# Kernel optimization log

Hardware: AMD Instinct MI355X
Metric: run time of the kernel (lower is better)

## Reference

```python
import jax, jax.numpy as jnp
import numpy as np

T, B, V, L = 512, 32, 512, 128
NEG = -1e9  # safe -inf surrogate (keeps logaddexp gradients finite)


def setup_inputs() -> dict:
    key = jax.random.key(0)
    k1, k2, k3 = jax.random.split(key, 3)
    log_probs = jax.nn.log_softmax(
        jax.random.normal(k1, (T, B, V), dtype=jnp.float32), axis=-1)
    # ASG transition parameter (init ones in the module; use small noise for a
    # non-degenerate reference). transition[i, j] = score of j -> i.
    transition = 0.1 * jax.random.normal(k2, (V, V), dtype=jnp.float32)
    targets = jax.random.randint(k3, (B, L), 0, V)
    input_lengths = jnp.full((B,), T, dtype=jnp.int32)
    target_lengths = jnp.full((B,), L, dtype=jnp.int32)
    return {"log_probs": log_probs, "transition": transition,
            "targets": targets, "input_lengths": input_lengths,
            "target_lengths": target_lengths}


def _fcc(log_probs, transition, input_lengths):
    """Fully-connected criterion: log-partition over all label paths. [B]"""
    def step(alpha, lp_t):  # alpha, lp_t: [B, V]
        # alpha'[b, i] = lp_t[b, i] + logsumexp_j(alpha[b, j] + trans[i, j])
        alpha = lp_t + jax.nn.logsumexp(
            alpha[:, None, :] + transition[None, :, :], axis=2)
        return alpha, jax.nn.logsumexp(alpha, axis=1)

    a0 = log_probs[0]
    _, tail = jax.lax.scan(step, a0, log_probs[1:])
    scores = jnp.concatenate(
        [jax.nn.logsumexp(a0, axis=1)[None], tail], axis=0)  # [T, B]
    return scores[input_lengths - 1, jnp.arange(scores.shape[1])]


def _fac(log_probs, transition, targets, input_lengths, target_lengths):
    """Forced-alignment criterion: DP constrained to the target label seq. [B]"""
    Tt, Bb, _ = log_probs.shape
    Ll = targets.shape[1]
    trans_self = transition[targets, targets]                    # [B, L] stay
    trans_prev = transition[targets[:, 1:], targets[:, :-1]]     # [B, L-1] advance
    # emit[t, b, s] = log_probs[t, b, targets[b, s]]
    emit = jnp.take_along_axis(
        log_probs, jnp.broadcast_to(targets[None], (Tt, Bb, Ll)), axis=2)

    sel = (target_lengths - 1)[:, None]  # [B, 1]

    def final_of(beta):
        return jnp.take_along_axis(beta, sel, axis=1)[:, 0]

    beta0 = jnp.where(jnp.arange(Ll)[None, :] == 0, emit[0], NEG)  # [B, L]

    def step(beta, em_t):
        stay = beta + trans_self
        move = jnp.concatenate(
            [jnp.full((Bb, 1), NEG, beta.dtype),
             beta[:, :-1] + trans_prev], axis=1)
        beta = em_t + jnp.logaddexp(stay, move)
        return beta, final_of(beta)

    _, tail = jax.lax.scan(step, beta0, emit[1:])
    fins = jnp.concatenate([final_of(beta0)[None], tail], axis=0)  # [T, B]
    return fins[input_lengths - 1, jnp.arange(Bb)]


def reference(log_probs, transition, targets, input_lengths, target_lengths):
    # ASG loss (reduction='none'): FCC - FAC, shape [B]
    fcc = _fcc(log_probs, transition, input_lengths)
    fac = _fac(log_probs, transition, targets, input_lengths, target_lengths)
    return fcc - fac
```

## Files before the change

### kernel.cpp

```cpp
#include <hip/hip_runtime.h>
#include <stdint.h>

#define T_ 512
#define B_ 32
#define V_ 512
#define L_ 128
#define NEGF (-1000000000.0f)

#define SE_Q 69.0f
#define SU_Q 127.0f
#define LOGC 9.078313f

typedef int v4i __attribute__((ext_vector_type(4)));

template <int CTRL>
__device__ __forceinline__ int dppmov(int old_, int src) {
    return __builtin_amdgcn_update_dpp(old_, src, CTRL, 0xF, 0xF, false);
}
__device__ __forceinline__ float wave_max64(float x) {
    int xi = __float_as_int(x);
    x = fmaxf(x, __int_as_float(dppmov<0x111>(xi, xi))); xi = __float_as_int(x);
    x = fmaxf(x, __int_as_float(dppmov<0x112>(xi, xi))); xi = __float_as_int(x);
    x = fmaxf(x, __int_as_float(dppmov<0x114>(xi, xi))); xi = __float_as_int(x);
    x = fmaxf(x, __int_as_float(dppmov<0x118>(xi, xi))); xi = __float_as_int(x);
    x = fmaxf(x, __int_as_float(dppmov<0x142>(xi, xi))); xi = __float_as_int(x);
    x = fmaxf(x, __int_as_float(dppmov<0x143>(xi, xi)));
    return x;
}
__device__ __forceinline__ float wave_sum64(float x) {
    int xi = __float_as_int(x);
    x = x + __int_as_float(dppmov<0x111>(xi, xi)); xi = __float_as_int(x);
    x = x + __int_as_float(dppmov<0x112>(xi, xi)); xi = __float_as_int(x);
    x = x + __int_as_float(dppmov<0x114>(xi, xi)); xi = __float_as_int(x);
    x = x + __int_as_float(dppmov<0x118>(xi, xi)); xi = __float_as_int(x);
    x = x + __int_as_float(dppmov<0x142>(xi, xi)); xi = __float_as_int(x);
    x = x + __int_as_float(dppmov<0x143>(xi, xi));
    return x;
}
__device__ __forceinline__ unsigned fkey(float f) {
    unsigned u = __float_as_uint(f);
    return (u & 0x80000000u) ? ~u : (u | 0x80000000u);
}
__device__ __forceinline__ float funkey(unsigned k) {
    unsigned u = (k & 0x80000000u) ? (k ^ 0x80000000u) : ~k;
    return __uint_as_float(u);
}
__device__ __forceinline__ int sel4(v4i a, int r) {
    int x0 = (r & 1) ? a.y : a.x;
    int x1 = (r & 1) ? a.w : a.z;
    return (r & 2) ? x1 : x0;
}

__global__ void asg_prep(const float* __restrict__ trans, uint32_t* __restrict__ Et) {
    int o = blockIdx.x * blockDim.x + threadIdx.x;
    int d    = o & 3;
    int tid  = (o >> 2) & 511;
    int qreg = o >> 11;
    int tt = qreg >> 3, kt = qreg & 7;
    int w = tid >> 6, lane = tid & 63;
    int q = lane >> 4, n = lane & 15;
    int m  = 64 * w + 16 * tt + n;
    int k0 = 64 * kt + 16 * q + 4 * d;
    const float* tp = trans + (size_t)m * V_ + k0;
    uint32_t q0 = (uint32_t)fminf(127.0f, __expf(tp[0]) * SE_Q + 0.5f);
    uint32_t q1 = (uint32_t)fminf(127.0f, __expf(tp[1]) * SE_Q + 0.5f);
    uint32_t q2 = (uint32_t)fminf(127.0f, __expf(tp[2]) * SE_Q + 0.5f);
    uint32_t q3 = (uint32_t)fminf(127.0f, __expf(tp[3]) * SE_Q + 0.5f);
    Et[(size_t)o] = q0 | (q1 << 8) | (q2 << 16) | (q3 << 24);
}

__global__ __attribute__((amdgpu_flat_work_group_size(512, 512),
                          amdgpu_waves_per_eu(2, 2)))
void asg_main(
    const float* __restrict__ lp, const uint32_t* __restrict__ Et,
    const float* __restrict__ trans, const int* __restrict__ targets,
    const int* __restrict__ ilen, const int* __restrict__ tlen,
    float* __restrict__ fcc_ws, float* __restrict__ fac_ws)
{
    __shared__ float facb[256];
    __shared__ __align__(16) uint32_t u_lds[128];
    __shared__ __align__(16) float mw_lds[8];
    __shared__ unsigned mslotE;
    __shared__ float sumf;

    const int bb  = blockIdx.x;
    const int tid = threadIdx.x;

    if (bb < B_) {
        const int b    = bb;
        const int lane = tid & 63;
        const int w    = tid >> 6;
        const int q    = lane >> 4;
        const int n    = lane & 15;
        const int tt_o = n >> 2;
        const int rg_o = n & 3;
        const int i    = 64 * w + 16 * tt_o + 4 * q + rg_o;
        const int Tlen = ilen[b];

        uint4 er4[32];
        {
            const uint4* Eq = (const uint4*)Et;
            #pragma unroll
            for (int t8 = 0; t8 < 32; ++t8) er4[t8] = Eq[t8 * 512 + tid];
        }

        float alpha = lp[(size_t)b * V_ + i];
        float lpv   = lp[(size_t)1 * (B_ * V_) + (size_t)b * V_ + i];
        if (tid == 0) { mslotE = 0u; sumf = 0.0f; }
        __syncthreads();

        for (int t = 1; t < Tlen; ++t) {
            {
                float mx = wave_max64(alpha);
                if (lane == 63) mw_lds[w] = mx;
            }
            __syncthreads();

            float4 m0 = *(const float4*)&mw_lds[0];
            float4 m1 = *(const float4*)&mw_lds[4];
            float m = fmaxf(fmaxf(fmaxf(m0.x, m0.y), fmaxf(m0.z, m0.w)),
                            fmaxf(fmaxf(m1.x, m1.y), fmaxf(m1.z, m1.w)));

            {
                float u = __expf(alpha - m);
                uint32_t qu = (uint32_t)(u * SU_Q + 0.5f);
                int pv = (int)(qu << (8 * (i & 3)));
                pv |= dppmov<0xB1>(pv, pv);
                pv |= dppmov<0x4E>(pv, pv);
                if ((i & 3) == 0) u_lds[i >> 2] = (uint32_t)pv;
            }
            __syncthreads();

            uint4 bf[8];
            #pragma unroll
            for (int kt = 0; kt < 8; ++kt)
                bf[kt] = *(const uint4*)((const char*)u_lds + 64 * kt + 16 * q);

            int tn = (t + 1 < Tlen) ? (t + 1) : t;
            float lpv_n = lp[(size_t)tn * (B_ * V_) + (size_t)b * V_ + i];

            v4i a0, a1, a2, a3;
            {
                v4i z = {0, 0, 0, 0};
                a0 = z; a1 = z; a2 = z; a3 = z;
            }
            #pragma unroll
            for (int kt = 0; kt < 8; ++kt) {
                v4i bv = __builtin_bit_cast(v4i, bf[kt]);
                a0 = __builtin_amdgcn_mfma_i32_16x16x64_i8(
                        __builtin_bit_cast(v4i, er4[0 * 8 + kt]), bv, a0, 0, 0, 0);
                a1 = __builtin_amdgcn_mfma_i32_16x16x64_i8(
                        __builtin_bit_cast(v4i, er4[1 * 8 + kt]), bv, a1, 0, 0, 0);
                a2 = __builtin_amdgcn_mfma_i32_16x16x64_i8(
                        __builtin_bit_cast(v4i, er4[2 * 8 + kt]), bv, a2, 0, 0, 0);
                a3 = __builtin_amdgcn_mfma_i32_16x16x64_i8(
                        __builtin_bit_cast(v4i, er4[3 * 8 + kt]), bv, a3, 0, 0, 0);
            }

            int s0 = sel4(a0, rg_o), s1 = sel4(a1, rg_o);
            int s2 = sel4(a2, rg_o), s3 = sel4(a3, rg_o);
            int y0 = (tt_o & 1) ? s1 : s0;
            int y1 = (tt_o & 1) ? s3 : s2;
            int acc = (tt_o & 2) ? y1 : y0;

            alpha = lpv + (m - LOGC) + __logf((float)acc);
            lpv = lpv_n;
        }

        {
            float mx = wave_max64(alpha);
            if (lane == 63) atomicMax(&mslotE, fkey(mx));
        }
        __syncthreads();
        float m2 = funkey(mslotE);
        {
            float sv = wave_sum64(__expf(alpha - m2));
            if (lane == 63) atomicAdd(&sumf, sv);
        }
        __syncthreads();
        if (tid == 0) fcc_ws[b] = m2 + __logf(sumf);
    } else {
        const int b = bb - B_;
        const int l = tid;
        const bool active = (l < L_);
        const int Tlen = ilen[b];
        const int Llen = tlen[b];

        const int tl  = active ? targets[b * L_ + l] : 0;
        const int tlm = (active && l > 0) ? targets[b * L_ + l - 1] : 0;
        const float ts = active ? trans[(size_t)tl * V_ + tl] : 0.0f;
        const float tp = (active && l > 0) ? trans[(size_t)tl * V_ + tlm] : 0.0f;

        float beta = (l == 0) ? lp[(size_t)b * V_ + tl] : NEGF;
        float em_next = active ? lp[(size_t)1 * (B_ * V_) + (size_t)b * V_ + tl] : 0.0f;

        for (int t = 1; t < Tlen; ++t) {
            float* buf = facb + (t & 1) * L_;
            if (active) buf[l] = beta;
            __syncthreads();
            float prev = (active && l > 0) ? buf[l - 1] : NEGF;
            float em = em_next;
            if (active && t + 1 < Tlen)
                em_next = lp[(size_t)(t + 1) * (B_ * V_) + (size_t)b * V_ + tl];
            if (active) {
                float st = beta + ts;
                float mv = prev + tp;
                float mx = fmaxf(st, mv);
                float mn = fminf(st, mv);
                beta = em + mx + log1pf(__expf(mn - mx));
            }
        }
        if (active && l == Llen - 1) fac_ws[b] = beta;
    }
}

__global__ void asg_combine(const float* __restrict__ fcc_ws,
                            const float* __restrict__ fac_ws,
                            float* __restrict__ out) {
    int i = threadIdx.x;
    if (i < B_) out[i] = fcc_ws[i] - fac_ws[i];
}

extern "C" void kernel_launch(void* const* d_in, const int* in_sizes, int n_in,
                              void* d_out, int out_size, void* d_ws, size_t ws_size,
                              hipStream_t stream) {
    const float* lp      = (const float*)d_in[0];
    const float* trans   = (const float*)d_in[1];
    const int*   targets = (const int*)d_in[2];
    const int*   ilen    = (const int*)d_in[3];
    const int*   tlen    = (const int*)d_in[4];
    float* out = (float*)d_out;

    uint32_t* Et     = (uint32_t*)d_ws;
    float*    fcc_ws = (float*)((char*)d_ws + 65536 * 4);
    float*    fac_ws = fcc_ws + B_;

    hipLaunchKernelGGL(asg_prep, dim3(256), dim3(256), 0, stream, trans, Et);
    hipLaunchKernelGGL(asg_main, dim3(2 * B_), dim3(512), 0, stream,
                       lp, Et, trans, targets, ilen, tlen, fcc_ws, fac_ws);
    hipLaunchKernelGGL(asg_combine, dim3(1), dim3(64), 0, stream, fcc_ws, fac_ws, out);
}
```

Before: 550.4 us.

## Run FCC recurrence in linear domain, fuse transition quantization, bpermute own k-tile

```diff
diff --git a/kernel.cpp b/kernel.cpp
--- a/kernel.cpp
+++ b/kernel.cpp
@@ -51,28 +51,10 @@
     return (r & 2) ? x1 : x0;
 }
 
-__global__ void asg_prep(const float* __restrict__ trans, uint32_t* __restrict__ Et) {
-    int o = blockIdx.x * blockDim.x + threadIdx.x;
-    int d    = o & 3;
-    int tid  = (o >> 2) & 511;
-    int qreg = o >> 11;
-    int tt = qreg >> 3, kt = qreg & 7;
-    int w = tid >> 6, lane = tid & 63;
-    int q = lane >> 4, n = lane & 15;
-    int m  = 64 * w + 16 * tt + n;
-    int k0 = 64 * kt + 16 * q + 4 * d;
-    const float* tp = trans + (size_t)m * V_ + k0;
-    uint32_t q0 = (uint32_t)fminf(127.0f, __expf(tp[0]) * SE_Q + 0.5f);
-    uint32_t q1 = (uint32_t)fminf(127.0f, __expf(tp[1]) * SE_Q + 0.5f);
-    uint32_t q2 = (uint32_t)fminf(127.0f, __expf(tp[2]) * SE_Q + 0.5f);
-    uint32_t q3 = (uint32_t)fminf(127.0f, __expf(tp[3]) * SE_Q + 0.5f);
-    Et[(size_t)o] = q0 | (q1 << 8) | (q2 << 16) | (q3 << 24);
-}
-
 __global__ __attribute__((amdgpu_flat_work_group_size(512, 512),
                           amdgpu_waves_per_eu(2, 2)))
 void asg_main(
-    const float* __restrict__ lp, const uint32_t* __restrict__ Et,
+    const float* __restrict__ lp,
     const float* __restrict__ trans, const int* __restrict__ targets,
     const int* __restrict__ ilen, const int* __restrict__ tlen,
     float* __restrict__ fcc_ws, float* __restrict__ fac_ws)
@@ -98,43 +80,74 @@
         const int Tlen = ilen[b];
 
         uint4 er4[32];
-        {
-            const uint4* Eq = (const uint4*)Et;
+        #pragma unroll
+        for (int tt = 0; tt < 4; ++tt) {
             #pragma unroll
-            for (int t8 = 0; t8 < 32; ++t8) er4[t8] = Eq[t8 * 512 + tid];
-        }
-
-        float alpha = lp[(size_t)b * V_ + i];
-        float lpv   = lp[(size_t)1 * (B_ * V_) + (size_t)b * V_ + i];
+            for (int s = 0; s < 8; ++s) {
+                int kt = (w + s) & 7;
+                const float* tp = trans + (size_t)(64 * w + 16 * tt + n) * V_
+                                        + 64 * kt + 16 * q;
+                uint32_t dw[4];
+                #pragma unroll
+                for (int d = 0; d < 4; ++d) {
+                    float4 tv = *(const float4*)(tp + 4 * d);
+                    uint32_t c0 = (uint32_t)fminf(127.0f, __expf(tv.x) * SE_Q + 0.5f);
+                    uint32_t c1 = (uint32_t)fminf(127.0f, __expf(tv.y) * SE_Q + 0.5f);
+                    uint32_t c2 = (uint32_t)fminf(127.0f, __expf(tv.z) * SE_Q + 0.5f);
+                    uint32_t c3 = (uint32_t)fminf(127.0f, __expf(tv.w) * SE_Q + 0.5f);
+                    dw[d] = c0 | (c1 << 8) | (c2 << 16) | (c3 << 24);
+                }
+                er4[tt * 8 + s].x = dw[0]; er4[tt * 8 + s].y = dw[1];
+                er4[tt * 8 + s].z = dw[2]; er4[tt * 8 + s].w = dw[3];
+            }
+        }
+
+        float lpv0 = lp[(size_t)b * V_ + i];
+        float elp  = __expf(lpv0);
+        float lpv  = lp[(size_t)(B_ * V_) + (size_t)b * V_ + i];
+        float accf = 1.0f;
+        float S    = 0.0f;
         if (tid == 0) { mslotE = 0u; sumf = 0.0f; }
         __syncthreads();
 
         for (int t = 1; t < Tlen; ++t) {
-            {
-                float mx = wave_max64(alpha);
+            float key = elp * accf;
+            float elp_n = __expf(lpv);
+
+            {
+                float mx = wave_max64(key);
                 if (lane == 63) mw_lds[w] = mx;
             }
             __syncthreads();
 
             float4 m0 = *(const float4*)&mw_lds[0];
             float4 m1 = *(const float4*)&mw_lds[4];
-            float m = fmaxf(fmaxf(fmaxf(m0.x, m0.y), fmaxf(m0.z, m0.w)),
-                            fmaxf(fmaxf(m1.x, m1.y), fmaxf(m1.z, m1.w)));
-
-            {
-                float u = __expf(alpha - m);
-                uint32_t qu = (uint32_t)(u * SU_Q + 0.5f);
-                int pv = (int)(qu << (8 * (i & 3)));
+            float kmax = fmaxf(fmaxf(fmaxf(m0.x, m0.y), fmaxf(m0.z, m0.w)),
+                               fmaxf(fmaxf(m1.x, m1.y), fmaxf(m1.z, m1.w)));
+            float r127 = 127.0f * __builtin_amdgcn_rcpf(kmax);
+
+            int pv;
+            {
+                uint32_t qu = (uint32_t)fminf(127.0f, fmaf(key, r127, 0.5f));
+                pv = (int)(qu << (8 * (i & 3)));
                 pv |= dppmov<0xB1>(pv, pv);
                 pv |= dppmov<0x4E>(pv, pv);
                 if ((i & 3) == 0) u_lds[i >> 2] = (uint32_t)pv;
             }
+
+            int bbase = lane & 48;
+            int ox = __builtin_amdgcn_ds_bpermute(bbase +   0, pv);
+            int oy = __builtin_amdgcn_ds_bpermute(bbase +  64, pv);
+            int oz = __builtin_amdgcn_ds_bpermute(bbase + 128, pv);
+            int ow = __builtin_amdgcn_ds_bpermute(bbase + 192, pv);
             __syncthreads();
 
-            uint4 bf[8];
+            uint4 bfr[7];
             #pragma unroll
-            for (int kt = 0; kt < 8; ++kt)
-                bf[kt] = *(const uint4*)((const char*)u_lds + 64 * kt + 16 * q);
+            for (int s = 1; s < 8; ++s) {
+                int kt = (w + s) & 7;
+                bfr[s - 1] = *(const uint4*)((const char*)u_lds + 64 * kt + 16 * q);
+            }
 
             int tn = (t + 1 < Tlen) ? (t + 1) : t;
             float lpv_n = lp[(size_t)tn * (B_ * V_) + (size_t)b * V_ + i];
@@ -144,17 +157,28 @@
                 v4i z = {0, 0, 0, 0};
                 a0 = z; a1 = z; a2 = z; a3 = z;
             }
+            {
+                v4i bv; bv.x = ox; bv.y = oy; bv.z = oz; bv.w = ow;
+                a0 = __builtin_amdgcn_mfma_i32_16x16x64_i8(
+                        __builtin_bit_cast(v4i, er4[0]),  bv, a0, 0, 0, 0);
+                a1 = __builtin_amdgcn_mfma_i32_16x16x64_i8(
+                        __builtin_bit_cast(v4i, er4[8]),  bv, a1, 0, 0, 0);
+                a2 = __builtin_amdgcn_mfma_i32_16x16x64_i8(
+                        __builtin_bit_cast(v4i, er4[16]), bv, a2, 0, 0, 0);
+                a3 = __builtin_amdgcn_mfma_i32_16x16x64_i8(
+                        __builtin_bit_cast(v4i, er4[24]), bv, a3, 0, 0, 0);
+            }
             #pragma unroll
-            for (int kt = 0; kt < 8; ++kt) {
-                v4i bv = __builtin_bit_cast(v4i, bf[kt]);
+            for (int s = 1; s < 8; ++s) {
+                v4i bv = __builtin_bit_cast(v4i, bfr[s - 1]);
                 a0 = __builtin_amdgcn_mfma_i32_16x16x64_i8(
-                        __builtin_bit_cast(v4i, er4[0 * 8 + kt]), bv, a0, 0, 0, 0);
+                        __builtin_bit_cast(v4i, er4[0 * 8 + s]), bv, a0, 0, 0, 0);
                 a1 = __builtin_amdgcn_mfma_i32_16x16x64_i8(
-                        __builtin_bit_cast(v4i, er4[1 * 8 + kt]), bv, a1, 0, 0, 0);
+                        __builtin_bit_cast(v4i, er4[1 * 8 + s]), bv, a1, 0, 0, 0);
                 a2 = __builtin_amdgcn_mfma_i32_16x16x64_i8(
-                        __builtin_bit_cast(v4i, er4[2 * 8 + kt]), bv, a2, 0, 0, 0);
+                        __builtin_bit_cast(v4i, er4[2 * 8 + s]), bv, a2, 0, 0, 0);
                 a3 = __builtin_amdgcn_mfma_i32_16x16x64_i8(
-                        __builtin_bit_cast(v4i, er4[3 * 8 + kt]), bv, a3, 0, 0, 0);
+                        __builtin_bit_cast(v4i, er4[3 * 8 + s]), bv, a3, 0, 0, 0);
             }
 
             int s0 = sel4(a0, rg_o), s1 = sel4(a1, rg_o);
@@ -163,10 +187,13 @@
             int y1 = (tt_o & 1) ? s3 : s2;
             int acc = (tt_o & 2) ? y1 : y0;
 
-            alpha = lpv + (m - LOGC) + __logf((float)acc);
+            accf = (float)acc;
+            S += __logf(kmax) - LOGC;
+            elp = elp_n;
             lpv = lpv_n;
         }
 
+        float alpha = ((Tlen > 1) ? lpv : lpv0) + S + __logf(accf);
         {
             float mx = wave_max64(alpha);
             if (lane == 63) atomicMax(&mslotE, fkey(mx));
@@ -231,12 +258,10 @@
     const int*   tlen    = (const int*)d_in[4];
     float* out = (float*)d_out;
 
-    uint32_t* Et     = (uint32_t*)d_ws;
-    float*    fcc_ws = (float*)((char*)d_ws + 65536 * 4);
-    float*    fac_ws = fcc_ws + B_;
-
-    hipLaunchKernelGGL(asg_prep, dim3(256), dim3(256), 0, stream, trans, Et);
+    float* fcc_ws = (float*)d_ws;
+    float* fac_ws = fcc_ws + B_;
+
     hipLaunchKernelGGL(asg_main, dim3(2 * B_), dim3(512), 0, stream,
-                       lp, Et, trans, targets, ilen, tlen, fcc_ws, fac_ws);
+                       lp, trans, targets, ilen, tlen, fcc_ws, fac_ws);
     hipLaunchKernelGGL(asg_combine, dim3(1), dim3(64), 0, stream, fcc_ws, fac_ws, out);
 }
```

Measured after the change: 615.8 us. 1.12x slower.

## Halve FCC workgroup to four waves, each handling two states

Applied to the files above, without the earlier changes.

```diff
diff --git a/kernel.cpp b/kernel.cpp
--- a/kernel.cpp
+++ b/kernel.cpp
@@ -45,21 +45,16 @@
     unsigned u = (k & 0x80000000u) ? (k ^ 0x80000000u) : ~k;
     return __uint_as_float(u);
 }
-__device__ __forceinline__ int sel4(v4i a, int r) {
-    int x0 = (r & 1) ? a.y : a.x;
-    int x1 = (r & 1) ? a.w : a.z;
-    return (r & 2) ? x1 : x0;
-}
 
 __global__ void asg_prep(const float* __restrict__ trans, uint32_t* __restrict__ Et) {
     int o = blockIdx.x * blockDim.x + threadIdx.x;
     int d    = o & 3;
-    int tid  = (o >> 2) & 511;
-    int qreg = o >> 11;
+    int tid  = (o >> 2) & 255;
+    int qreg = o >> 10;
     int tt = qreg >> 3, kt = qreg & 7;
     int w = tid >> 6, lane = tid & 63;
     int q = lane >> 4, n = lane & 15;
-    int m  = 64 * w + 16 * tt + n;
+    int m  = 128 * w + 16 * tt + n;
     int k0 = 64 * kt + 16 * q + 4 * d;
     const float* tp = trans + (size_t)m * V_ + k0;
     uint32_t q0 = (uint32_t)fminf(127.0f, __expf(tp[0]) * SE_Q + 0.5f);
@@ -69,8 +64,8 @@
     Et[(size_t)o] = q0 | (q1 << 8) | (q2 << 16) | (q3 << 24);
 }
 
-__global__ __attribute__((amdgpu_flat_work_group_size(512, 512),
-                          amdgpu_waves_per_eu(2, 2)))
+__global__ __attribute__((amdgpu_flat_work_group_size(256, 256),
+                          amdgpu_waves_per_eu(1, 1)))
 void asg_main(
     const float* __restrict__ lp, const uint32_t* __restrict__ Et,
     const float* __restrict__ trans, const int* __restrict__ targets,
@@ -79,7 +74,7 @@
 {
     __shared__ float facb[256];
     __shared__ __align__(16) uint32_t u_lds[128];
-    __shared__ __align__(16) float mw_lds[8];
+    __shared__ __align__(16) float mw_lds[4];
     __shared__ unsigned mslotE;
     __shared__ float sumf;
 
@@ -92,42 +87,43 @@
         const int w    = tid >> 6;
         const int q    = lane >> 4;
         const int n    = lane & 15;
-        const int tt_o = n >> 2;
-        const int rg_o = n & 3;
-        const int i    = 64 * w + 16 * tt_o + 4 * q + rg_o;
+        const int tt_o = n >> 1;
+        const int i0   = 128 * w + 16 * tt_o + 4 * q + 2 * (n & 1);
         const int Tlen = ilen[b];
 
-        uint4 er4[32];
+        uint4 er[64];
         {
             const uint4* Eq = (const uint4*)Et;
             #pragma unroll
-            for (int t8 = 0; t8 < 32; ++t8) er4[t8] = Eq[t8 * 512 + tid];
-        }
-
-        float alpha = lp[(size_t)b * V_ + i];
-        float lpv   = lp[(size_t)1 * (B_ * V_) + (size_t)b * V_ + i];
+            for (int j = 0; j < 64; ++j) er[j] = Eq[j * 256 + tid];
+        }
+
+        float2 a0v = *(const float2*)&lp[(size_t)b * V_ + i0];
+        float alpha0 = a0v.x, alpha1 = a0v.y;
+        float2 lv = *(const float2*)&lp[(size_t)(B_ * V_) + (size_t)b * V_ + i0];
+        float lpv0 = lv.x, lpv1 = lv.y;
         if (tid == 0) { mslotE = 0u; sumf = 0.0f; }
         __syncthreads();
 
         for (int t = 1; t < Tlen; ++t) {
             {
-                float mx = wave_max64(alpha);
+                float mx = wave_max64(fmaxf(alpha0, alpha1));
                 if (lane == 63) mw_lds[w] = mx;
             }
             __syncthreads();
 
-            float4 m0 = *(const float4*)&mw_lds[0];
-            float4 m1 = *(const float4*)&mw_lds[4];
-            float m = fmaxf(fmaxf(fmaxf(m0.x, m0.y), fmaxf(m0.z, m0.w)),
-                            fmaxf(fmaxf(m1.x, m1.y), fmaxf(m1.z, m1.w)));
+            float4 mq = *(const float4*)&mw_lds[0];
+            float m = fmaxf(fmaxf(mq.x, mq.y), fmaxf(mq.z, mq.w));
 
             {
-                float u = __expf(alpha - m);
-                uint32_t qu = (uint32_t)(u * SU_Q + 0.5f);
-                int pv = (int)(qu << (8 * (i & 3)));
-                pv |= dppmov<0xB1>(pv, pv);
-                pv |= dppmov<0x4E>(pv, pv);
-                if ((i & 3) == 0) u_lds[i >> 2] = (uint32_t)pv;
+                float u0 = __expf(alpha0 - m);
+                float u1 = __expf(alpha1 - m);
+                uint32_t q0 = (uint32_t)(u0 * SU_Q + 0.5f);
+                uint32_t q1 = (uint32_t)(u1 * SU_Q + 0.5f);
+                int u16o = (int)(q0 | (q1 << 8));
+                int pr = dppmov<0xB1>(u16o, u16o);
+                if ((n & 1) == 0)
+                    u_lds[32 * w + 4 * (n >> 1) + q] = (uint32_t)(u16o | (pr << 16));
             }
             __syncthreads();
 
@@ -137,44 +133,68 @@
                 bf[kt] = *(const uint4*)((const char*)u_lds + 64 * kt + 16 * q);
 
             int tn = (t + 1 < Tlen) ? (t + 1) : t;
-            float lpv_n = lp[(size_t)tn * (B_ * V_) + (size_t)b * V_ + i];
-
-            v4i a0, a1, a2, a3;
+            float2 lvn = *(const float2*)&lp[(size_t)tn * (B_ * V_) + (size_t)b * V_ + i0];
+
+            v4i A0, A1, A2, A3, A4, A5, A6, A7;
             {
                 v4i z = {0, 0, 0, 0};
-                a0 = z; a1 = z; a2 = z; a3 = z;
+                A0 = z; A1 = z; A2 = z; A3 = z; A4 = z; A5 = z; A6 = z; A7 = z;
             }
             #pragma unroll
             for (int kt = 0; kt < 8; ++kt) {
                 v4i bv = __builtin_bit_cast(v4i, bf[kt]);
-                a0 = __builtin_amdgcn_mfma_i32_16x16x64_i8(
-                        __builtin_bit_cast(v4i, er4[0 * 8 + kt]), bv, a0, 0, 0, 0);
-                a1 = __builtin_amdgcn_mfma_i32_16x16x64_i8(
-                        __builtin_bit_cast(v4i, er4[1 * 8 + kt]), bv, a1, 0, 0, 0);
-                a2 = __builtin_amdgcn_mfma_i32_16x16x64_i8(
-                        __builtin_bit_cast(v4i, er4[2 * 8 + kt]), bv, a2, 0, 0, 0);
-                a3 = __builtin_amdgcn_mfma_i32_16x16x64_i8(
-                        __builtin_bit_cast(v4i, er4[3 * 8 + kt]), bv, a3, 0, 0, 0);
-            }
-
-            int s0 = sel4(a0, rg_o), s1 = sel4(a1, rg_o);
-            int s2 = sel4(a2, rg_o), s3 = sel4(a3, rg_o);
-            int y0 = (tt_o & 1) ? s1 : s0;
-            int y1 = (tt_o & 1) ? s3 : s2;
-            int acc = (tt_o & 2) ? y1 : y0;
-
-            alpha = lpv + (m - LOGC) + __logf((float)acc);
-            lpv = lpv_n;
+                A0 = __builtin_amdgcn_mfma_i32_16x16x64_i8(
+                        __builtin_bit_cast(v4i, er[0 * 8 + kt]), bv, A0, 0, 0, 0);
+                A1 = __builtin_amdgcn_mfma_i32_16x16x64_i8(
+                        __builtin_bit_cast(v4i, er[1 * 8 + kt]), bv, A1, 0, 0, 0);
+                A2 = __builtin_amdgcn_mfma_i32_16x16x64_i8(
+                        __builtin_bit_cast(v4i, er[2 * 8 + kt]), bv, A2, 0, 0, 0);
+                A3 = __builtin_amdgcn_mfma_i32_16x16x64_i8(
+                        __builtin_bit_cast(v4i, er[3 * 8 + kt]), bv, A3, 0, 0, 0);
+                A4 = __builtin_amdgcn_mfma_i32_16x16x64_i8(
+                        __builtin_bit_cast(v4i, er[4 * 8 + kt]), bv, A4, 0, 0, 0);
+                A5 = __builtin_amdgcn_mfma_i32_16x16x64_i8(
+                        __builtin_bit_cast(v4i, er[5 * 8 + kt]), bv, A5, 0, 0, 0);
+                A6 = __builtin_amdgcn_mfma_i32_16x16x64_i8(
+                        __builtin_bit_cast(v4i, er[6 * 8 + kt]), bv, A6, 0, 0, 0);
+                A7 = __builtin_amdgcn_mfma_i32_16x16x64_i8(
+                        __builtin_bit_cast(v4i, er[7 * 8 + kt]), bv, A7, 0, 0, 0);
+            }
+
+            const bool nb = (n & 1) != 0;
+            int p00 = nb ? A0.z : A0.x, p10 = nb ? A0.w : A0.y;
+            int p01 = nb ? A1.z : A1.x, p11 = nb ? A1.w : A1.y;
+            int p02 = nb ? A2.z : A2.x, p12 = nb ? A2.w : A2.y;
+            int p03 = nb ? A3.z : A3.x, p13 = nb ? A3.w : A3.y;
+            int p04 = nb ? A4.z : A4.x, p14 = nb ? A4.w : A4.y;
+            int p05 = nb ? A5.z : A5.x, p15 = nb ? A5.w : A5.y;
+            int p06 = nb ? A6.z : A6.x, p16 = nb ? A6.w : A6.y;
+            int p07 = nb ? A7.z : A7.x, p17 = nb ? A7.w : A7.y;
+            const bool t0b = (tt_o & 1) != 0;
+            const bool t1b = (tt_o & 2) != 0;
+            const bool t2b = (tt_o & 4) != 0;
+            int q00 = t0b ? p01 : p00, q01 = t0b ? p03 : p02;
+            int q02 = t0b ? p05 : p04, q03 = t0b ? p07 : p06;
+            int q10 = t0b ? p11 : p10, q11 = t0b ? p13 : p12;
+            int q12 = t0b ? p15 : p14, q13 = t0b ? p17 : p16;
+            int r00 = t1b ? q01 : q00, r01 = t1b ? q03 : q02;
+            int r10 = t1b ? q11 : q10, r11 = t1b ? q13 : q12;
+            int acc0 = t2b ? r01 : r00;
+            int acc1 = t2b ? r11 : r10;
+
+            alpha0 = lpv0 + (m - LOGC) + __logf((float)acc0);
+            alpha1 = lpv1 + (m - LOGC) + __logf((float)acc1);
+            lpv0 = lvn.x; lpv1 = lvn.y;
         }
 
         {
-            float mx = wave_max64(alpha);
+            float mx = wave_max64(fmaxf(alpha0, alpha1));
             if (lane == 63) atomicMax(&mslotE, fkey(mx));
         }
         __syncthreads();
         float m2 = funkey(mslotE);
         {
-            float sv = wave_sum64(__expf(alpha - m2));
+            float sv = wave_sum64(__expf(alpha0 - m2) + __expf(alpha1 - m2));
             if (lane == 63) atomicAdd(&sumf, sv);
         }
         __syncthreads();
@@ -236,7 +256,7 @@
     float*    fac_ws = fcc_ws + B_;
 
     hipLaunchKernelGGL(asg_prep, dim3(256), dim3(256), 0, stream, trans, Et);
-    hipLaunchKernelGGL(asg_main, dim3(2 * B_), dim3(512), 0, stream,
+    hipLaunchKernelGGL(asg_main, dim3(2 * B_), dim3(256), 0, stream,
                        lp, Et, trans, targets, ilen, tlen, fcc_ws, fac_ws);
     hipLaunchKernelGGL(asg_combine, dim3(1), dim3(64), 0, stream, fcc_ws, fac_ws, out);
 }
```

Result: slower. 682.6 us (+24.0%).

## Fuse prep, main and combine kernels into one launch with global flag sync

Applied to the files above, without the earlier changes.

```diff
diff --git a/kernel.cpp b/kernel.cpp
--- a/kernel.cpp
+++ b/kernel.cpp
@@ -51,31 +51,19 @@
     return (r & 2) ? x1 : x0;
 }
 
-__global__ void asg_prep(const float* __restrict__ trans, uint32_t* __restrict__ Et) {
-    int o = blockIdx.x * blockDim.x + threadIdx.x;
-    int d    = o & 3;
-    int tid  = (o >> 2) & 511;
-    int qreg = o >> 11;
-    int tt = qreg >> 3, kt = qreg & 7;
-    int w = tid >> 6, lane = tid & 63;
-    int q = lane >> 4, n = lane & 15;
-    int m  = 64 * w + 16 * tt + n;
-    int k0 = 64 * kt + 16 * q + 4 * d;
-    const float* tp = trans + (size_t)m * V_ + k0;
-    uint32_t q0 = (uint32_t)fminf(127.0f, __expf(tp[0]) * SE_Q + 0.5f);
-    uint32_t q1 = (uint32_t)fminf(127.0f, __expf(tp[1]) * SE_Q + 0.5f);
-    uint32_t q2 = (uint32_t)fminf(127.0f, __expf(tp[2]) * SE_Q + 0.5f);
-    uint32_t q3 = (uint32_t)fminf(127.0f, __expf(tp[3]) * SE_Q + 0.5f);
-    Et[(size_t)o] = q0 | (q1 << 8) | (q2 << 16) | (q3 << 24);
-}
+#define WS_ET_DW     65536
+#define WS_FAC_OFF   262144
+#define WS_FLAG_OFF  262272
 
 __global__ __attribute__((amdgpu_flat_work_group_size(512, 512),
                           amdgpu_waves_per_eu(2, 2)))
-void asg_main(
-    const float* __restrict__ lp, const uint32_t* __restrict__ Et,
+void asg_fused(
+    const float* __restrict__ lp,
     const float* __restrict__ trans, const int* __restrict__ targets,
     const int* __restrict__ ilen, const int* __restrict__ tlen,
-    float* __restrict__ fcc_ws, float* __restrict__ fac_ws)
+    uint32_t* __restrict__ Et, float* __restrict__ fac_ws,
+    unsigned* __restrict__ prep_done, unsigned* __restrict__ fac_flag,
+    float* __restrict__ out)
 {
     __shared__ float facb[256];
     __shared__ __align__(16) uint32_t u_lds[128];
@@ -97,6 +85,13 @@
         const int i    = 64 * w + 16 * tt_o + 4 * q + rg_o;
         const int Tlen = ilen[b];
 
+        if (tid == 0) {
+            while (atomicAdd(prep_done, 0u) < 32u) __builtin_amdgcn_s_sleep(2);
+            mslotE = 0u; sumf = 0.0f;
+        }
+        __syncthreads();
+        __threadfence();
+
         uint4 er4[32];
         {
             const uint4* Eq = (const uint4*)Et;
@@ -106,7 +101,6 @@
 
         float alpha = lp[(size_t)b * V_ + i];
         float lpv   = lp[(size_t)1 * (B_ * V_) + (size_t)b * V_ + i];
-        if (tid == 0) { mslotE = 0u; sumf = 0.0f; }
         __syncthreads();
 
         for (int t = 1; t < Tlen; ++t) {
@@ -178,9 +172,37 @@
             if (lane == 63) atomicAdd(&sumf, sv);
         }
         __syncthreads();
-        if (tid == 0) fcc_ws[b] = m2 + __logf(sumf);
+        if (tid == 0) {
+            float fcc = m2 + __logf(sumf);
+            while (atomicAdd(&fac_flag[b], 0u) == 0u) __builtin_amdgcn_s_sleep(2);
+            __threadfence();
+            out[b] = fcc - fac_ws[b];
+        }
     } else {
         const int b = bb - B_;
+
+        #pragma unroll
+        for (int k = 0; k < 4; ++k) {
+            int o = b * 2048 + k * 512 + tid;
+            int d    = o & 3;
+            int ptid = (o >> 2) & 511;
+            int qreg = o >> 11;
+            int tt = qreg >> 3, kt = qreg & 7;
+            int pw = ptid >> 6, plane = ptid & 63;
+            int pq = plane >> 4, pn = plane & 15;
+            int m  = 64 * pw + 16 * tt + pn;
+            int k0 = 64 * kt + 16 * pq + 4 * d;
+            const float* tp = trans + (size_t)m * V_ + k0;
+            uint32_t q0 = (uint32_t)fminf(127.0f, __expf(tp[0]) * SE_Q + 0.5f);
+            uint32_t q1 = (uint32_t)fminf(127.0f, __expf(tp[1]) * SE_Q + 0.5f);
+            uint32_t q2 = (uint32_t)fminf(127.0f, __expf(tp[2]) * SE_Q + 0.5f);
+            uint32_t q3 = (uint32_t)fminf(127.0f, __expf(tp[3]) * SE_Q + 0.5f);
+            Et[(size_t)o] = q0 | (q1 << 8) | (q2 << 16) | (q3 << 24);
+        }
+        __threadfence();
+        __syncthreads();
+        if (tid == 0) atomicAdd(prep_done, 1u);
+
         const int l = tid;
         const bool active = (l < L_);
         const int Tlen = ilen[b];
@@ -210,15 +232,12 @@
                 beta = em + mx + log1pf(__expf(mn - mx));
             }
         }
-        if (active && l == Llen - 1) fac_ws[b] = beta;
+        if (active && l == Llen - 1) {
+            fac_ws[b] = beta;
+            __threadfence();
+            atomicExch(&fac_flag[b], 1u);
+        }
     }
-}
-
-__global__ void asg_combine(const float* __restrict__ fcc_ws,
-                            const float* __restrict__ fac_ws,
-                            float* __restrict__ out) {
-    int i = threadIdx.x;
-    if (i < B_) out[i] = fcc_ws[i] - fac_ws[i];
 }
 
 extern "C" void kernel_launch(void* const* d_in, const int* in_sizes, int n_in,
@@ -231,12 +250,14 @@
     const int*   tlen    = (const int*)d_in[4];
     float* out = (float*)d_out;
 
-    uint32_t* Et     = (uint32_t*)d_ws;
-    float*    fcc_ws = (float*)((char*)d_ws + 65536 * 4);
-    float*    fac_ws = fcc_ws + B_;
-
-    hipLaunchKernelGGL(asg_prep, dim3(256), dim3(256), 0, stream, trans, Et);
-    hipLaunchKernelGGL(asg_main, dim3(2 * B_), dim3(512), 0, stream,
-                       lp, Et, trans, targets, ilen, tlen, fcc_ws, fac_ws);
-    hipLaunchKernelGGL(asg_combine, dim3(1), dim3(64), 0, stream, fcc_ws, fac_ws, out);
-}
+    uint32_t* Et        = (uint32_t*)d_ws;
+    float*    fac_ws    = (float*)((char*)d_ws + WS_FAC_OFF);
+    unsigned* prep_done = (unsigned*)((char*)d_ws + WS_FLAG_OFF);
+    unsigned* fac_flag  = prep_done + 1;
+
+    hipMemsetAsync((char*)d_ws + WS_FLAG_OFF, 0, 256, stream);
+
+    hipLaunchKernelGGL(asg_fused, dim3(2 * B_), dim3(512), 0, stream,
+                       lp, trans, targets, ilen, tlen,
+                       Et, fac_ws, prep_done, fac_flag, out);
+}
```

Measured after the change: 572.9 us. 1.04x slower.
